# Kernel optimization log

Hardware: AMD Instinct MI355X
Metric: run time of the kernel (lower is better)

Reference implementation:

```python
import jax, jax.numpy as jnp
import numpy as np

# YOLOLayer config (matches init_kwargs)
ANCHORS = [(0.1, 0.13), (0.3, 0.35), (0.6, 0.55)]  # (w, h) as fraction of image
NUM_CLASSES = 80
STRIDE = 8
NA = len(ANCHORS)


def setup_inputs() -> dict:
    key = jax.random.key(0)
    B, C, G = 16, NA * (NUM_CLASSES + 5), 64
    x = jax.random.normal(key, (B, C, G, G), dtype=jnp.float32)
    return {"x": x}


def reference(x):
    B = x.shape[0]
    g0, g1 = x.shape[2], x.shape[3]
    nC = NUM_CLASSES
    # [B, nA, g0, g1, 5+nC]
    pred = x.reshape(B, NA, nC + 5, g0, g1).transpose(0, 1, 3, 4, 2)
    sx = jax.nn.sigmoid(pred[..., 0])
    sy = jax.nn.sigmoid(pred[..., 1])
    w = pred[..., 2]
    h = pred[..., 3]
    pred_conf = jax.nn.sigmoid(pred[..., 4])
    pred_cls = jax.nn.sigmoid(pred[..., 5:])

    # grid offsets: grid_x varies along last dim, grid_y along dim -2 (torch semantics)
    grid_x = jnp.arange(g1, dtype=x.dtype)[None, None, None, :]
    grid_y = jnp.arange(g0, dtype=x.dtype)[None, None, :, None]
    scaled = jnp.asarray([(aw * g0, ah * g1) for aw, ah in ANCHORS], dtype=x.dtype)
    anchor_w = scaled[:, 0].reshape(1, NA, 1, 1)
    anchor_h = scaled[:, 1].reshape(1, NA, 1, 1)

    # torch uses .data (detached) for pred_boxes -> stop_gradient for faithfulness
    pred_boxes = jnp.stack(
        [sx + grid_x, sy + grid_y, jnp.exp(w) * anchor_w, jnp.exp(h) * anchor_h],
        axis=-1,
    )
    pred_boxes = jax.lax.stop_gradient(pred_boxes)

    boxes = pred_boxes.reshape(B, -1, 4) * STRIDE
    conf = pred_conf.reshape(B, -1, 1)
    cls = pred_cls.reshape(B, -1, nC)
    return boxes, conf, cls
```

## Files before the change

kernel.cpp:

```cpp
#include <hip/hip_runtime.h>


#define NB 16
#define NA 3
#define NC 80
#define GG 4096
#define CH 85
#define S  128

__device__ __forceinline__ float sigmoidf(float v) {
    return 1.0f / (1.0f + __expf(-v));
}

__device__ __forceinline__ int lidx(int ch, int p) {
    int g = (p >> 2) ^ ((ch >> 2) & 7);
    return ch * S + (g << 2) + (p & 3);
}

__global__ __launch_bounds__(512) void yolo_kernel(const float* __restrict__ x,
                                                   float* __restrict__ out) {
    __shared__ float lds[CH * S];

    const int tilesPer = GG / S;
    int blk  = blockIdx.x;
    int tile = blk & (tilesPer - 1);
    int ba   = blk / tilesPer;
    int a    = ba % NA;
    int s0   = tile * S;

    const float4* __restrict__ xin4 =
        reinterpret_cast<const float4*>(x + (size_t)ba * CH * GG + s0);
    for (int i = threadIdx.x; i < CH * (S / 4); i += 512) {
        int ch = i >> 5;
        int p4 = i & 31;
        int g  = p4 ^ ((ch >> 2) & 7);
        float4 v = xin4[ch * (GG / 4) + p4];
        *reinterpret_cast<float4*>(&lds[ch * S + (g << 2)]) = v;
    }
    __syncthreads();

    const float anchor_w[NA] = {0.1f * 64 * 8, 0.3f * 64 * 8, 0.6f * 64 * 8};
    const float anchor_h[NA] = {0.13f * 64 * 8, 0.35f * 64 * 8, 0.55f * 64 * 8};

    const int loc = ba * GG + s0;
    float* __restrict__ boxes = out;
    float* __restrict__ conf  = out + (size_t)NB * NA * GG * 4;
    float* __restrict__ cls   = out + (size_t)NB * NA * GG * 5;

    if (threadIdx.x < S) {
        int p  = threadIdx.x;
        int sp = s0 + p;
        float gx = (float)(sp & 63);
        float gy = (float)(sp >> 6);
        float4 bx;
        bx.x = (sigmoidf(lds[lidx(0, p)]) + gx) * 8.0f;
        bx.y = (sigmoidf(lds[lidx(1, p)]) + gy) * 8.0f;
        bx.z = __expf(lds[lidx(2, p)]) * anchor_w[a];
        bx.w = __expf(lds[lidx(3, p)]) * anchor_h[a];
        reinterpret_cast<float4*>(boxes)[loc + p] = bx;
        conf[loc + p] = sigmoidf(lds[lidx(4, p)]);
    }

    float4* __restrict__ cls4 =
        reinterpret_cast<float4*>(cls + (size_t)loc * NC);
    for (int i = threadIdx.x; i < NC * (S / 4); i += 512) {
        int p  = i / 20;
        int c4 = i % 20;
        int r  = 5 + (c4 << 2);
        float4 v;
        v.x = sigmoidf(lds[lidx(r + 0, p)]);
        v.y = sigmoidf(lds[lidx(r + 1, p)]);
        v.z = sigmoidf(lds[lidx(r + 2, p)]);
        v.w = sigmoidf(lds[lidx(r + 3, p)]);
        cls4[i] = v;
    }
}

extern "C" void kernel_launch(void* const* d_in, const int* in_sizes, int n_in,
                              void* d_out, int out_size, void* d_ws, size_t ws_size,
                              hipStream_t stream) {
    const float* x = (const float*)d_in[0];
    float* out = (float*)d_out;
    dim3 grid(NB * NA * (GG / S));
    yolo_kernel<<<grid, 512, 0, stream>>>(x, out);
}
```

Measured before the change: 27.44 us.

## Load input tile directly to LDS via global_load_lds with smaller tiles

Swaps the register-staged float4 global-to-LDS copy for direct global_load_lds DMA-style loads. It also halves the spatial tile to 64 positions with 256-thread blocks, which doubles the block count and halves LDS per block. The goal is to cut VGPR round-trips and raise occupancy and memory-level parallelism. The swizzle moves from the LDS write side to the global read addresses, which relies on each wave's 64 contiguous LDS slots mapping correctly.

```diff
diff --git a/kernel.cpp b/kernel.cpp
--- a/kernel.cpp
+++ b/kernel.cpp
@@ -1,4 +1,5 @@
 #include <hip/hip_runtime.h>
+#include <stdint.h>
 
 
 #define NB 16
@@ -6,7 +7,8 @@
 #define NC 80
 #define GG 4096
 #define CH 85
-#define S  128
+#define S  64
+#define NG (CH * (S / 4))
 
 __device__ __forceinline__ float sigmoidf(float v) {
     return 1.0f / (1.0f + __expf(-v));
@@ -14,28 +16,39 @@
 
 __device__ __forceinline__ int lidx(int ch, int p) {
     int g = (p >> 2) ^ ((ch >> 2) & 7);
-    return ch * S + (g << 2) + (p & 3);
+    return (ch << 6) + (g << 2) + (p & 3);
 }
 
-__global__ __launch_bounds__(512) void yolo_kernel(const float* __restrict__ x,
+__global__ __launch_bounds__(256) void yolo_kernel(const float* __restrict__ x,
                                                    float* __restrict__ out) {
     __shared__ float lds[CH * S];
 
-    const int tilesPer = GG / S;
-    int blk  = blockIdx.x;
-    int tile = blk & (tilesPer - 1);
-    int ba   = blk / tilesPer;
-    int a    = ba % NA;
-    int s0   = tile * S;
+    const int blk  = blockIdx.x;
+    const int tile = blk & 63;
+    const int ba   = blk >> 6;
+    const int a    = ba % NA;
+    const int s0   = tile * S;
+    const int tid  = threadIdx.x;
+    const int lane = tid & 63;
+    const int wv   = tid >> 6;
 
-    const float4* __restrict__ xin4 =
-        reinterpret_cast<const float4*>(x + (size_t)ba * CH * GG + s0);
-    for (int i = threadIdx.x; i < CH * (S / 4); i += 512) {
-        int ch = i >> 5;
-        int p4 = i & 31;
-        int g  = p4 ^ ((ch >> 2) & 7);
-        float4 v = xin4[ch * (GG / 4) + p4];
-        *reinterpret_cast<float4*>(&lds[ch * S + (g << 2)]) = v;
+    const float* __restrict__ xin = x + (size_t)ba * CH * GG + s0;
+
+    #pragma unroll
+    for (int it = 0; it < 6; ++it) {
+        int g0 = it * 256 + wv * 64;
+        int g  = g0 + lane;
+        if (g < NG) {
+            int ch  = g >> 4;
+            int p4  = g & 15;
+            int sp4 = p4 ^ ((ch >> 2) & 7);
+            const float* gp = xin + (size_t)ch * GG + (sp4 << 2);
+            float* lp = &lds[g0 << 2];
+            __builtin_amdgcn_global_load_lds(
+                (const __attribute__((address_space(1))) void*)gp,
+                (__attribute__((address_space(3))) void*)lp,
+                16, 0, 0);
+        }
     }
     __syncthreads();
 
@@ -47,8 +60,8 @@
     float* __restrict__ conf  = out + (size_t)NB * NA * GG * 4;
     float* __restrict__ cls   = out + (size_t)NB * NA * GG * 5;
 
-    if (threadIdx.x < S) {
-        int p  = threadIdx.x;
+    if (tid < S) {
+        int p  = tid;
         int sp = s0 + p;
         float gx = (float)(sp & 63);
         float gy = (float)(sp >> 6);
@@ -62,8 +75,9 @@
     }
 
     float4* __restrict__ cls4 =
-        reinterpret_cast<float4*>(cls + (size_t)loc * NC);
-    for (int i = threadIdx.x; i < NC * (S / 4); i += 512) {
+        reinterpret_cast<float4*>(cls) + (size_t)loc * 20;
+    #pragma unroll
+    for (int i = tid; i < (S * 20); i += 256) {
         int p  = i / 20;
         int c4 = i % 20;
         int r  = 5 + (c4 << 2);
@@ -82,5 +96,5 @@
     const float* x = (const float*)d_in[0];
     float* out = (float*)d_out;
     dim3 grid(NB * NA * (GG / S));
-    yolo_kernel<<<grid, 512, 0, stream>>>(x, out);
+    yolo_kernel<<<grid, 256, 0, stream>>>(x, out);
 }
```

After: 25.83 us. -5.9%, faster.
